# Kernel tuning notes

Hardware: AMD Instinct MI355X
Metric: run time of the kernel (lower is better)

The kernel has to match this reference:

```python
import jax, jax.numpy as jnp
import numpy as np

NUM_HEADS = 8
SPLIT_S = 4
DIM = 288            # n_feat * 3 * 3
SCALE = (DIM // NUM_HEADS) ** -0.5  # quirk: uses full dim's head_dim (36), not reduced
EPS = 1e-5


def _extract_patches(x):
    # x: [B,C,H,W] -> [B, C*9, H*W], 3x3 kernel, stride 1, 'same' padding
    B, C, H, W = x.shape
    xp = jnp.pad(x, ((0, 0), (0, 0), (1, 1), (1, 1)))
    pats = jnp.stack([xp[:, :, i:i + H, j:j + W] for i in range(3) for j in range(3)], axis=2)
    return pats.reshape(B, C * 9, H * W)


def _fold(cols, H, W):
    # inverse of extract: [B, C*9, H*W] -> [B,C,H,W], summing overlapping patches
    B, Ck, _ = cols.shape
    C = Ck // 9
    p = cols.reshape(B, C, 3, 3, H, W)
    out = jnp.zeros((B, C, H + 2, W + 2), cols.dtype)
    for i in range(3):
        for j in range(3):
            out = out.at[:, :, i:i + H, j:j + W].add(p[:, :, i, j])
    return out[:, :, 1:H + 1, 1:W + 1]


def _ln(x, w, b):
    mu = x.mean(-1, keepdims=True)
    var = ((x - mu) ** 2).mean(-1, keepdims=True)
    return (x - mu) * jax.lax.rsqrt(var + EPS) * w + b


def _attn(x, reduce_w, qkv_w, proj_w, proj_b):
    # x: [B,N,288] -> reduce -> [B,N,144] -> block-diag attention over s=4 chunks
    x = x @ reduce_w.T
    B, N, C = x.shape
    hd = C // NUM_HEADS
    qkv = (x @ qkv_w.T).reshape(B, N, 3, NUM_HEADS, hd).transpose(2, 0, 3, 1, 4)
    q, k, v = qkv[0], qkv[1], qkv[2]          # [B,h,N,hd]
    chunk = N // SPLIT_S
    q = q.reshape(B, NUM_HEADS, SPLIT_S, chunk, hd)
    k = k.reshape(B, NUM_HEADS, SPLIT_S, chunk, hd)
    v = v.reshape(B, NUM_HEADS, SPLIT_S, chunk, hd)
    attn = jnp.einsum('bhscd,bhsed->bhsce', q, k) * SCALE   # [B,h,s,chunk,chunk]
    attn = jax.nn.softmax(attn, axis=-1)
    out = jnp.einsum('bhsce,bhsed->bhscd', attn, v)          # [B,h,s,chunk,hd]
    out = out.transpose(0, 2, 3, 1, 4).reshape(B, N, C)      # cat chunks on token dim
    return out @ proj_w.T + proj_b


def setup_inputs() -> dict:
    key = jax.random.key(0)
    ks = jax.random.split(key, 12)
    d, dr, dh = DIM, DIM // 2, DIM // 4  # 288, 144, 72
    f = lambda k, shape: (jax.random.normal(k, shape, jnp.float32) * 0.02)
    return {
        'x': jax.random.normal(ks[0], (4, 32, 64, 64), jnp.float32),
        'ln1_w': jnp.ones((d,), jnp.float32), 'ln1_b': jnp.zeros((d,), jnp.float32),
        'reduce_w': f(ks[1], (dr, d)),
        'qkv_w': f(ks[2], (3 * dr, dr)),
        'proj_w': f(ks[3], (d, dr)), 'proj_b': jnp.zeros((d,), jnp.float32),
        'ln2_w': jnp.ones((d,), jnp.float32), 'ln2_b': jnp.zeros((d,), jnp.float32),
        'fc1_w': f(ks[4], (dh, d)), 'fc1_b': jnp.zeros((dh,), jnp.float32),
        'fc2_w': f(ks[5], (d, dh)), 'fc2_b': jnp.zeros((d,), jnp.float32),
    }


def reference(x, ln1_w, ln1_b, reduce_w, qkv_w, proj_w, proj_b, ln2_w, ln2_b, fc1_w, fc1_b, fc2_w, fc2_b):
    B, C, H, W = x.shape
    t = _extract_patches(x).transpose(0, 2, 1)  # [B, N=H*W, 288]
    t = t + _attn(_ln(t, ln1_w, ln1_b), reduce_w, qkv_w, proj_w, proj_b)
    h = _ln(t, ln2_w, ln2_b)
    t = t + (jax.nn.relu(h @ fc1_w.T + fc1_b) @ fc2_w.T + fc2_b)
    return _fold(t.transpose(0, 2, 1), H, W)
```

## Files before the change

kernel.cpp:

```cpp
#include <hip/hip_runtime.h>
#include <hip/hip_bf16.h>

typedef __hip_bfloat16 bf16;
typedef unsigned short u16;
typedef unsigned int u32;
typedef __attribute__((ext_vector_type(8))) short bf16x8;
typedef __attribute__((ext_vector_type(4))) float f32x4;

#define BB 4
#define CCH 32
#define HH 64
#define WW 64
#define NN 4096
#define D 288
#define DR 144
#define DQ 432
#define NH 8
#define HD 18
#define SPLIT 4
#define CHUNK 1024
#define KS 512
#define DH 72
#define SCALE_ 0.16666666666666666f
#define QSCALE 0.24044917348149343f
#define EPS_ 1e-5f
#define ASTR 160
#define ATS 168
#define HSTR 96

__device__ __attribute__((aligned(16))) u16 g_Wcb[DQ * D];
__device__ __attribute__((aligned(16))) u16 g_pw[D * ASTR];
__device__ __attribute__((aligned(16))) u16 g_f1w[HSTR * D];
__device__ __attribute__((aligned(16))) u16 g_f2w[D * HSTR];
__device__ __attribute__((aligned(16))) u16 g_q[(size_t)BB * NH * NN * 32];
__device__ __attribute__((aligned(16))) u16 g_k[(size_t)BB * NH * NN * 32];
__device__ __attribute__((aligned(16))) u16 g_vt[(size_t)BB * NH * SPLIT * 32 * CHUNK];
__device__ __attribute__((aligned(16))) float g_part[2 * (size_t)BB * NH * NN * 20];
__device__ __attribute__((aligned(16))) u16 g_t0[(size_t)BB * NN * D];
__device__ __attribute__((aligned(16))) u16 g_t2b[(size_t)BB * D * NN];
__device__ int   g_flag;

__device__ __forceinline__ float b2f(bf16 v) { return __bfloat162float(v); }
__device__ __forceinline__ float bits2f(u16 u) { return __uint_as_float(((u32)u) << 16); }
__device__ __forceinline__ u16 f2bits(float f) {
    u32 u = __float_as_uint(f);
    return (u16)((u + 0x7FFF + ((u >> 16) & 1)) >> 16);
}
__device__ __forceinline__ float ldin(const void* p, size_t i, int isbf) {
    return isbf ? b2f(((const bf16*)p)[i]) : ((const float*)p)[i];
}

#define RS  (D * ASTR + HSTR * D + D * HSTR)
#define RS2 (RS + BB * NH * SPLIT * CHUNK)
#define RSB ((RS2 + 255) / 256)
#define PATCHB (BB * HH)

__global__ void k_prep(const void* __restrict__ x, const void* __restrict__ qkv_w,
                       const void* __restrict__ reduce_w, const void* __restrict__ proj_w,
                       const void* __restrict__ fc1_w, const void* __restrict__ fc2_w) {
    __shared__ int cnt4[4];
    __shared__ float qw[DR];
    __shared__ float slab[32 * 3 * 66];
    int tid = threadIdx.x;
    {
        const u16* u = (const u16*)x;
        int c = 0;
        for (int i = tid; i < 2048; i += 256) c += (((u[i] >> 7) & 0xFF) >= 0x90);
        for (int o = 32; o; o >>= 1) c += __shfl_xor(c, o);
        if ((tid & 63) == 0) cnt4[tid >> 6] = c;
    }
    __syncthreads();
    int bf = (cnt4[0] + cnt4[1] + cnt4[2] + cnt4[3]) < 32;
    if (tid == 0 && blockIdx.x == 0) g_flag = bf;

    int bid = blockIdx.x;
    if (bid < DQ) {
        int o = bid;
        if (tid < DR) qw[tid] = ldin(qkv_w, (size_t)o * DR + tid, bf);
        __syncthreads();
        for (int col = tid; col < D; col += 256) {
            float s0 = 0.f, s1 = 0.f;
            #pragma unroll 4
            for (int j = 0; j < DR; j += 2) {
                s0 += qw[j] * ldin(reduce_w, (size_t)j * D + col, bf);
                s1 += qw[j + 1] * ldin(reduce_w, (size_t)(j + 1) * D + col, bf);
            }
            g_Wcb[(size_t)o * D + col] = f2bits(s0 + s1);
        }
    } else if (bid < DQ + RSB) {
        int idx = (bid - DQ) * 256 + tid;
        if (idx < D * ASTR) {
            int o = idx / ASTR, j = idx % ASTR;
            g_pw[idx] = (j < DR) ? f2bits(ldin(proj_w, (size_t)o * DR + j, bf)) : (u16)0;
        } else if (idx < D * ASTR + HSTR * D) {
            int t = idx - D * ASTR;
            int o = t / D;
            g_f1w[t] = (o < DH) ? f2bits(ldin(fc1_w, (size_t)t, bf)) : (u16)0;
        } else if (idx < RS) {
            int t = idx - D * ASTR - HSTR * D;
            int o = t / HSTR, j = t % HSTR;
            g_f2w[t] = (j < DH) ? f2bits(ldin(fc2_w, (size_t)o * DH + j, bf)) : (u16)0;
        } else if (idx < RS2) {
            int t = idx - RS;
            int bhs = t >> 10, n = t & 1023;
            g_vt[((size_t)bhs * 32 + 18) * CHUNK + n] = 0x3F80;
        }
    } else {
        int pb = bid - DQ - RSB;
        int b = pb >> 6, y = pb & 63;
        for (int idx = tid; idx < 32 * 3 * 66; idx += 256) {
            int c = idx / 198, rem = idx % 198;
            int ki = rem / 66, col = rem % 66 - 1;
            int sy = y + ki - 1;
            float v = 0.f;
            if (col >= 0 && col < 64 && sy >= 0 && sy < 64)
                v = ldin(x, ((size_t)(b * CCH + c) * HH + sy) * WW + col, bf);
            slab[idx] = v;
        }
        __syncthreads();
        size_t obase = ((size_t)b * NN + y * 64) * D;
        for (int idx = tid; idx < 64 * D; idx += 256) {
            int t = idx / D, f = idx % D;
            int c = f / 9, k = f % 9, ki = k / 3, kj = k % 3;
            g_t0[obase + idx] = f2bits(slab[c * 198 + ki * 66 + t + kj]);
        }
    }
}

__global__ void k_ln_qkv(const void* __restrict__ lnw, const void* __restrict__ lnb) {
    __shared__ __attribute__((aligned(16))) u16 xln[32 * 296];
    __shared__ float lnwf[D], lnbf[D];
    __shared__ float smu[32], srs[32];
    __shared__ u16 buf[3][144][32];
    int bf = g_flag;
    int tid = threadIdx.x;
    size_t tok0 = (size_t)blockIdx.x * 32;
    for (int i = tid; i < D; i += 256) { lnwf[i] = ldin(lnw, i, bf); lnbf[i] = ldin(lnb, i, bf); }
    {
        int tt = tid >> 3, p = tid & 7;
        const u32* pr = (const u32*)(g_t0 + (tok0 + tt) * D + p * 36);
        float s = 0.f, q = 0.f;
        #pragma unroll
        for (int j = 0; j < 18; ++j) {
            u32 v = pr[j];
            float a = bits2f((u16)(v & 0xFFFF)), b = bits2f((u16)(v >> 16));
            s += a + b; q += a * a + b * b;
        }
        #pragma unroll
        for (int o = 1; o < 8; o <<= 1) { s += __shfl_xor(s, o); q += __shfl_xor(q, o); }
        if (p == 0) {
            float mu = s / D;
            smu[tt] = mu;
            srs[tt] = rsqrtf(q / D - mu * mu + EPS_);
        }
    }
    __syncthreads();
    for (int idx = tid; idx < 32 * 144; idx += 256) {
        int t = idx / 144, dw = idx % 144;
        u32 v = *(const u32*)(g_t0 + (tok0 + t) * D + 2 * dw);
        float mu = smu[t], rs = srs[t];
        int f = 2 * dw;
        float a = (bits2f((u16)(v & 0xFFFF)) - mu) * rs * lnwf[f] + lnbf[f];
        float b = (bits2f((u16)(v >> 16)) - mu) * rs * lnwf[f + 1] + lnbf[f + 1];
        *(u32*)&xln[t * 296 + f] = (u32)f2bits(a) | ((u32)f2bits(b) << 16);
    }
    __syncthreads();
    int w = tid >> 6, lane = tid & 63, quad = lane >> 4, l15 = lane & 15;
    bf16x8 areg0[9], areg1[9];
    {
        const u16* a0 = xln + l15 * 296 + quad * 8;
        const u16* a1 = xln + (16 + l15) * 296 + quad * 8;
        #pragma unroll
        for (int ks = 0; ks < 9; ++ks) {
            areg0[ks] = *(const bf16x8*)(a0 + ks * 32);
            areg1[ks] = *(const bf16x8*)(a1 + ks * 32);
        }
    }
    int nt0 = w * 7, nt1 = (nt0 + 7 > 27) ? 27 : nt0 + 7;
    for (int nt = nt0; nt < nt1; ++nt) {
        f32x4 acc0 = {0.f, 0.f, 0.f, 0.f}, acc1 = {0.f, 0.f, 0.f, 0.f};
        const u16* bbase = g_Wcb + (size_t)(nt * 16 + l15) * D + quad * 8;
        #pragma unroll
        for (int ks = 0; ks < 9; ++ks) {
            bf16x8 bfr = *(const bf16x8*)(bbase + ks * 32);
            acc0 = __builtin_amdgcn_mfma_f32_16x16x32_bf16(areg0[ks], bfr, acc0, 0, 0, 0);
            acc1 = __builtin_amdgcn_mfma_f32_16x16x32_bf16(areg1[ks], bfr, acc1, 0, 0, 0);
        }
        int o = nt * 16 + l15;
        int which = o / DR, rem = o % DR;
        #pragma unroll
        for (int r = 0; r < 4; ++r) {
            buf[which][rem][quad * 4 + r] = f2bits(which == 0 ? acc0[r] * QSCALE : acc0[r]);
            buf[which][rem][16 + quad * 4 + r] = f2bits(which == 0 ? acc1[r] * QSCALE : acc1[r]);
        }
    }
    __syncthreads();
    {
        int b_ = (int)(tok0 >> 12);
        int n0 = (int)(tok0 & 4095);
        int sIdx = n0 >> 10, nc = n0 & 1023;
        for (int idx = tid; idx < 2 * 8 * 32 * 9; idx += 256) {
            int which = idx / 2304;
            int r2 = idx - which * 2304;
            int h = r2 / 288, r3 = r2 % 288, t = r3 / 9, dw = r3 % 9;
            u32 lo = buf[which][h * 18 + 2 * dw][t];
            u32 hi = buf[which][h * 18 + 2 * dw + 1][t];
            u16* dst = (which ? g_k : g_q) + ((size_t)(b_ * NH + h) * NN + n0 + t) * 32 + 2 * dw;
            *(u32*)dst = lo | (hi << 16);
        }
        for (int idx = tid; idx < 144 * 16; idx += 256) {
            int rem = idx >> 4, tp = idx & 15;
            int hh = rem / HD, dd = rem % HD;
            u32 lo = buf[2][rem][2 * tp];
            u32 hi = buf[2][rem][2 * tp + 1];
            size_t voff = (((size_t)(b_ * NH + hh) * SPLIT + sIdx) * 32 + dd) * CHUNK + nc + 2 * tp;
            *(u32*)&g_vt[voff] = lo | (hi << 16);
        }
    }
}

#define PSTR 72
__global__ __launch_bounds__(128) void k_attn() {
    __shared__ __attribute__((aligned(16))) u16 Pl[2][4][16 * PSTR];
    int bid = blockIdx.x;
    int chunk = bid & 127;
    int qblk = (bid >> 7) & 7;
    int ksl = bid >> 10;
    int s = chunk & 3, bh = chunk >> 2;
    int tid = threadIdx.x;
    int w = tid >> 6, lane = tid & 63, quad = lane >> 4, l15 = lane & 15;

    size_t rowbase = (size_t)bh * NN + s * CHUNK;
    size_t vtbase = ((size_t)bh * SPLIT + s) * 32 * CHUNK;
    const u16* kbase = g_k + rowbase * 32 + quad * 8;
    const u16* vbase = g_vt + vtbase + quad * 8;

    int qbase = qblk * 128 + w * 64;
    bf16x8 qf[4];
    #pragma unroll
    for (int t = 0; t < 4; ++t)
        qf[t] = *(const bf16x8*)(g_q + (rowbase + qbase + t * 16 + l15) * 32 + quad * 8);

    f32x4 accA[4], accB[4];
    #pragma unroll
    for (int t = 0; t < 4; ++t) {
        accA[t] = (f32x4){0.f, 0.f, 0.f, 0.f};
        accB[t] = (f32x4){0.f, 0.f, 0.f, 0.f};
    }

    int kt0 = ksl * KS;
    for (int kk = 0; kk < KS; kk += 64) {
        int kt = kt0 + kk;
        bf16x8 kf0 = *(const bf16x8*)(kbase + (size_t)(kt + 2 * l15) * 32);
        bf16x8 kf1 = *(const bf16x8*)(kbase + (size_t)(kt + 2 * l15 + 1) * 32);
        bf16x8 kf2 = *(const bf16x8*)(kbase + (size_t)(kt + 32 + 2 * l15) * 32);
        bf16x8 kf3 = *(const bf16x8*)(kbase + (size_t)(kt + 33 + 2 * l15) * 32);
        bf16x8 vA0 = *(const bf16x8*)(vbase + (size_t)l15 * CHUNK + kt);
        bf16x8 vB0 = *(const bf16x8*)(vbase + (size_t)(16 + l15) * CHUNK + kt);
        bf16x8 vA1 = *(const bf16x8*)(vbase + (size_t)l15 * CHUNK + kt + 32);
        bf16x8 vB1 = *(const bf16x8*)(vbase + (size_t)(16 + l15) * CHUNK + kt + 32);
        f32x4 z = {0.f, 0.f, 0.f, 0.f};
        #pragma unroll
        for (int t = 0; t < 4; ++t) {
            u16* pw = Pl[w][t];
            f32x4 S0 = __builtin_amdgcn_mfma_f32_16x16x32_bf16(qf[t], kf0, z, 0, 0, 0);
            f32x4 S1 = __builtin_amdgcn_mfma_f32_16x16x32_bf16(qf[t], kf1, z, 0, 0, 0);
            f32x4 S2 = __builtin_amdgcn_mfma_f32_16x16x32_bf16(qf[t], kf2, z, 0, 0, 0);
            f32x4 S3 = __builtin_amdgcn_mfma_f32_16x16x32_bf16(qf[t], kf3, z, 0, 0, 0);
            #pragma unroll
            for (int r = 0; r < 4; ++r) {
                float p0 = exp2f(S0[r]), p1 = exp2f(S1[r]);
                float p2 = exp2f(S2[r]), p3 = exp2f(S3[r]);
                u32 w0 = __builtin_amdgcn_perm(__float_as_uint(p1), __float_as_uint(p0), 0x07060302u);
                u32 w1 = __builtin_amdgcn_perm(__float_as_uint(p3), __float_as_uint(p2), 0x07060302u);
                *(u32*)&pw[(quad * 4 + r) * PSTR + 2 * l15] = w0;
                *(u32*)&pw[(quad * 4 + r) * PSTR + 32 + 2 * l15] = w1;
            }
        }
        #pragma unroll
        for (int t = 0; t < 4; ++t) {
            const u16* pw = Pl[w][t];
            bf16x8 pf0 = *(const bf16x8*)&pw[l15 * PSTR + quad * 8];
            bf16x8 pf1 = *(const bf16x8*)&pw[l15 * PSTR + 32 + quad * 8];
            accA[t] = __builtin_amdgcn_mfma_f32_16x16x32_bf16(pf0, vA0, accA[t], 0, 0, 0);
            accB[t] = __builtin_amdgcn_mfma_f32_16x16x32_bf16(pf0, vB0, accB[t], 0, 0, 0);
            accA[t] = __builtin_amdgcn_mfma_f32_16x16x32_bf16(pf1, vA1, accA[t], 0, 0, 0);
            accB[t] = __builtin_amdgcn_mfma_f32_16x16x32_bf16(pf1, vB1, accB[t], 0, 0, 0);
        }
    }
    float* pb = g_part + (((size_t)ksl * 32 + bh) * SPLIT + s) * (size_t)(CHUNK * 20);
    #pragma unroll
    for (int t = 0; t < 4; ++t) {
        #pragma unroll
        for (int r = 0; r < 4; ++r) {
            int tokenc = qbase + t * 16 + quad * 4 + r;
            float* row = pb + (size_t)tokenc * 20;
            row[l15] = accA[t][r];
            if (l15 < 3) row[16 + l15] = accB[t][r];
        }
    }
}

__global__ void k_proj_mlp(const void* __restrict__ proj_b, const void* __restrict__ lnw,
                           const void* __restrict__ lnb, const void* __restrict__ fc1_b,
                           const void* __restrict__ fc2_b) {
    __shared__ __attribute__((aligned(16))) u16 t1f[32 * 296];
    __shared__ __attribute__((aligned(16))) u16 xln[32 * 296];
    __shared__ __attribute__((aligned(16))) u16 attnT[32 * ATS];
    __shared__ __attribute__((aligned(16))) u16 hbuf[32 * HSTR];
    __shared__ float lnwf[D], lnbf[D];
    __shared__ float smu[32], srs[32];
    int bf = g_flag;
    int tid = threadIdx.x;
    size_t tok0 = (size_t)blockIdx.x * 32;
    int w = tid >> 6, lane = tid & 63, quad = lane >> 4, l15 = lane & 15;
    for (int i = tid; i < D; i += 256) { lnwf[i] = ldin(lnw, i, bf); lnbf[i] = ldin(lnb, i, bf); }

    int b_ = (int)(tok0 >> 12);
    int s_ = ((int)tok0 & 4095) >> 10;
    int tc0 = (int)tok0 & 1023;
    for (int idx = tid; idx < 32 * (ATS - DR); idx += 256) {
        int t = idx / (ATS - DR), f = idx % (ATS - DR);
        attnT[t * ATS + DR + f] = 0;
    }
    {
        int t = tid >> 3, h = tid & 7;
        const float* p1 = g_part + (((size_t)(b_ * NH + h)) * SPLIT + s_) * (size_t)(CHUNK * 20)
                        + (size_t)(tc0 + t) * 20;
        const float* p2 = p1 + (size_t)32 * SPLIT * CHUNK * 20;
        f32x4 a0 = *(const f32x4*)p1,        c0 = *(const f32x4*)p2;
        f32x4 a1 = *(const f32x4*)(p1 + 4),  c1 = *(const f32x4*)(p2 + 4);
        f32x4 a2 = *(const f32x4*)(p1 + 8),  c2 = *(const f32x4*)(p2 + 8);
        f32x4 a3 = *(const f32x4*)(p1 + 12), c3 = *(const f32x4*)(p2 + 12);
        f32x4 a4 = *(const f32x4*)(p1 + 16), c4 = *(const f32x4*)(p2 + 16);
        float inv = 1.f / (a4[2] + c4[2]);
        u16* dst = attnT + t * ATS + h * HD;
        #pragma unroll
        for (int d = 0; d < 4; ++d) {
            dst[d]      = f2bits((a0[d] + c0[d]) * inv);
            dst[4 + d]  = f2bits((a1[d] + c1[d]) * inv);
            dst[8 + d]  = f2bits((a2[d] + c2[d]) * inv);
            dst[12 + d] = f2bits((a3[d] + c3[d]) * inv);
        }
        dst[16] = f2bits((a4[0] + c4[0]) * inv);
        dst[17] = f2bits((a4[1] + c4[1]) * inv);
    }
    __syncthreads();

    {
        bf16x8 areg0[5], areg1[5];
        const u16* a0 = attnT + l15 * ATS + quad * 8;
        const u16* a1 = attnT + (16 + l15) * ATS + quad * 8;
        #pragma unroll
        for (int ks = 0; ks < 5; ++ks) {
            areg0[ks] = *(const bf16x8*)(a0 + ks * 32);
            areg1[ks] = *(const bf16x8*)(a1 + ks * 32);
        }
        const int tab[5] = {0, 5, 10, 14, 18};
        for (int nt = tab[w]; nt < tab[w + 1]; ++nt) {
            f32x4 acc0 = {0.f, 0.f, 0.f, 0.f}, acc1 = {0.f, 0.f, 0.f, 0.f};
            const u16* bbase = g_pw + (size_t)(nt * 16 + l15) * ASTR + quad * 8;
            #pragma unroll
            for (int ks = 0; ks < 5; ++ks) {
                bf16x8 bfr = *(const bf16x8*)(bbase + ks * 32);
                acc0 = __builtin_amdgcn_mfma_f32_16x16x32_bf16(areg0[ks], bfr, acc0, 0, 0, 0);
                acc1 = __builtin_amdgcn_mfma_f32_16x16x32_bf16(areg1[ks], bfr, acc1, 0, 0, 0);
            }
            int o = nt * 16 + l15;
            float bias = ldin(proj_b, o, bf);
            #pragma unroll
            for (int r = 0; r < 4; ++r) {
                t1f[(quad * 4 + r) * 296 + o] =
                    f2bits(bits2f(g_t0[(tok0 + quad * 4 + r) * D + o]) + acc0[r] + bias);
                t1f[(16 + quad * 4 + r) * 296 + o] =
                    f2bits(bits2f(g_t0[(tok0 + 16 + quad * 4 + r) * D + o]) + acc1[r] + bias);
            }
        }
    }
    __syncthreads();
    {
        int tt = tid >> 3, p = tid & 7;
        const u32* src = (const u32*)&t1f[tt * 296 + p * 36];
        float s = 0.f, q = 0.f;
        #pragma unroll
        for (int j = 0; j < 18; ++j) {
            u32 v = src[j];
            float a = bits2f((u16)(v & 0xFFFF)), b = bits2f((u16)(v >> 16));
            s += a + b; q += a * a + b * b;
        }
        #pragma unroll
        for (int o = 1; o < 8; o <<= 1) { s += __shfl_xor(s, o); q += __shfl_xor(q, o); }
        if (p == 0) {
            float mu = s / D;
            smu[tt] = mu;
            srs[tt] = rsqrtf(q / D - mu * mu + EPS_);
        }
    }
    __syncthreads();
    for (int idx = tid; idx < 32 * 144; idx += 256) {
        int t = idx / 144, dw = idx % 144;
        int f = 2 * dw;
        u32 v = *(const u32*)&t1f[t * 296 + f];
        float mu = smu[t], rs = srs[t];
        float a = (bits2f((u16)(v & 0xFFFF)) - mu) * rs * lnwf[f] + lnbf[f];
        float b = (bits2f((u16)(v >> 16)) - mu) * rs * lnwf[f + 1] + lnbf[f + 1];
        *(u32*)&xln[t * 296 + f] = (u32)f2bits(a) | ((u32)f2bits(b) << 16);
    }
    __syncthreads();
    {
        bf16x8 areg0[9], areg1[9];
        const u16* a0 = xln + l15 * 296 + quad * 8;
        const u16* a1 = xln + (16 + l15) * 296 + quad * 8;
        #pragma unroll
        for (int ks = 0; ks < 9; ++ks) {
            areg0[ks] = *(const bf16x8*)(a0 + ks * 32);
            areg1[ks] = *(const bf16x8*)(a1 + ks * 32);
        }
        const int tab2[5] = {0, 2, 4, 5, 6};
        for (int nt = tab2[w]; nt < tab2[w + 1]; ++nt) {
            f32x4 acc0 = {0.f, 0.f, 0.f, 0.f}, acc1 = {0.f, 0.f, 0.f, 0.f};
            const u16* bbase = g_f1w + (size_t)(nt * 16 + l15) * D + quad * 8;
            #pragma unroll
            for (int ks = 0; ks < 9; ++ks) {
                bf16x8 bfr = *(const bf16x8*)(bbase + ks * 32);
                acc0 = __builtin_amdgcn_mfma_f32_16x16x32_bf16(areg0[ks], bfr, acc0, 0, 0, 0);
                acc1 = __builtin_amdgcn_mfma_f32_16x16x32_bf16(areg1[ks], bfr, acc1, 0, 0, 0);
            }
            int o = nt * 16 + l15;
            float bias = (o < DH) ? ldin(fc1_b, o, bf) : 0.f;
            #pragma unroll
            for (int r = 0; r < 4; ++r) {
                hbuf[(quad * 4 + r) * HSTR + o] = f2bits(fmaxf(acc0[r] + bias, 0.f));
                hbuf[(16 + quad * 4 + r) * HSTR + o] = f2bits(fmaxf(acc1[r] + bias, 0.f));
            }
        }
    }
    __syncthreads();
    {
        bf16x8 areg0[3], areg1[3];
        const u16* a0 = hbuf + l15 * HSTR + quad * 8;
        const u16* a1 = hbuf + (16 + l15) * HSTR + quad * 8;
        #pragma unroll
        for (int ks = 0; ks < 3; ++ks) {
            areg0[ks] = *(const bf16x8*)(a0 + ks * 32);
            areg1[ks] = *(const bf16x8*)(a1 + ks * 32);
        }
        const int tab[5] = {0, 5, 10, 14, 18};
        for (int nt = tab[w]; nt < tab[w + 1]; ++nt) {
            f32x4 acc0 = {0.f, 0.f, 0.f, 0.f}, acc1 = {0.f, 0.f, 0.f, 0.f};
            const u16* bbase = g_f2w + (size_t)(nt * 16 + l15) * HSTR + quad * 8;
            #pragma unroll
            for (int ks = 0; ks < 3; ++ks) {
                bf16x8 bfr = *(const bf16x8*)(bbase + ks * 32);
                acc0 = __builtin_amdgcn_mfma_f32_16x16x32_bf16(areg0[ks], bfr, acc0, 0, 0, 0);
                acc1 = __builtin_amdgcn_mfma_f32_16x16x32_bf16(areg1[ks], bfr, acc1, 0, 0, 0);
            }
            int o = nt * 16 + l15;
            float bias = ldin(fc2_b, o, bf);
            #pragma unroll
            for (int r = 0; r < 4; ++r) {
                xln[(quad * 4 + r) * 296 + o] =
                    f2bits(bits2f(t1f[(quad * 4 + r) * 296 + o]) + acc0[r] + bias);
                xln[(16 + quad * 4 + r) * 296 + o] =
                    f2bits(bits2f(t1f[(16 + quad * 4 + r) * 296 + o]) + acc1[r] + bias);
            }
        }
    }
    __syncthreads();
    {
        int n0 = (int)(tok0 & 4095);
        for (int idx = tid; idx < D * 16; idx += 256) {
            int o = idx >> 4, tp = idx & 15;
            u32 v = (u32)xln[(2 * tp) * 296 + o] | ((u32)xln[(2 * tp + 1) * 296 + o] << 16);
            *(u32*)&g_t2b[((size_t)b_ * D + o) * NN + n0 + 2 * tp] = v;
        }
    }
}

__global__ void k_fold(void* __restrict__ out) {
    int bf = g_flag;
    int idx = blockIdx.x * blockDim.x + threadIdx.x;
    if (idx >= BB * CCH * HH * WW) return;
    int xx = idx % WW;
    int y = (idx / WW) % HH;
    int c = (idx / (WW * HH)) % CCH;
    int b = idx / (WW * HH * CCH);
    const u16* base = g_t2b + ((size_t)b * D + c * 9) * NN;
    float s = 0.f;
    #pragma unroll
    for (int i = 0; i < 3; ++i) {
        int sy = y + 1 - i;
        if (sy < 0 || sy >= HH) continue;
        #pragma unroll
        for (int j = 0; j < 3; ++j) {
            int sx = xx + 1 - j;
            if (sx < 0 || sx >= WW) continue;
            s += bits2f(base[(size_t)(i * 3 + j) * NN + sy * WW + sx]);
        }
    }
    if (bf) ((bf16*)out)[idx] = __float2bfloat16(s);
    else    ((float*)out)[idx] = s;
}

extern "C" void kernel_launch(void* const* d_in, const int* in_sizes, int n_in,
                              void* d_out, int out_size, void* d_ws, size_t ws_size,
                              hipStream_t stream) {
    const void* x        = d_in[0];
    const void* ln1_w    = d_in[1];
    const void* ln1_b    = d_in[2];
    const void* reduce_w = d_in[3];
    const void* qkv_w    = d_in[4];
    const void* proj_w   = d_in[5];
    const void* proj_b   = d_in[6];
    const void* ln2_w    = d_in[7];
    const void* ln2_b    = d_in[8];
    const void* fc1_w    = d_in[9];
    const void* fc1_b    = d_in[10];
    const void* fc2_w    = d_in[11];
    const void* fc2_b    = d_in[12];

    k_prep     <<<DQ + RSB + PATCHB, 256, 0, stream>>>(x, qkv_w, reduce_w, proj_w, fc1_w, fc2_w);
    k_ln_qkv   <<<BB * NN / 32, 256, 0, stream>>>(ln1_w, ln1_b);
    k_attn     <<<2 * BB * NH * SPLIT * 8, 128, 0, stream>>>();
    k_proj_mlp <<<BB * NN / 32, 256, 0, stream>>>(proj_b, ln2_w, ln2_b, fc1_b, fc2_b);
    k_fold     <<<(BB * CCH * HH * WW + 255) / 256, 256, 0, stream>>>(d_out);
}
```

Before: 200.0 us.

## Keep attention probabilities in registers by transposing S and permuting V layout

The QK^T MFMA now computes S transposed (K as the A operand), so each lane's accumulator values line up with the A-operand layout needed for the PV MFMA. The exponentials are packed straight into bf16x8 registers instead of going through a shared-memory staging buffer. To match, the V^T producer writes keys in a permuted order within each 32-key group. This removes the LDS writes, reads and their latency from the attention inner loop and adds a launch-bounds occupancy hint, at the cost of a more fragile layout coupling between the producer and the consumer kernel.

Result: no change. 197.1 us (-1.4%).

```diff
diff --git a/kernel.cpp b/kernel.cpp
--- a/kernel.cpp
+++ b/kernel.cpp
@@ -49,6 +49,10 @@
 __device__ __forceinline__ float ldin(const void* p, size_t i, int isbf) {
     return isbf ? b2f(((const bf16*)p)[i]) : ((const float*)p)[i];
 }
+__device__ __forceinline__ u32 packexp(float e0, float e1) {
+    return __builtin_amdgcn_perm(__float_as_uint(exp2f(e1)),
+                                 __float_as_uint(exp2f(e0)), 0x07060302u);
+}
 
 #define RS  (D * ASTR + HSTR * D + D * HSTR)
 #define RS2 (RS + BB * NH * SPLIT * CHUNK)
@@ -213,15 +217,15 @@
             int hh = rem / HD, dd = rem % HD;
             u32 lo = buf[2][rem][2 * tp];
             u32 hi = buf[2][rem][2 * tp + 1];
-            size_t voff = (((size_t)(b_ * NH + hh) * SPLIT + sIdx) * 32 + dd) * CHUNK + nc + 2 * tp;
+            int k2 = 2 * tp;
+            int pos = 8 * ((k2 >> 2) & 3) + 4 * (k2 >> 4) + (k2 & 3);
+            size_t voff = (((size_t)(b_ * NH + hh) * SPLIT + sIdx) * 32 + dd) * CHUNK + nc + pos;
             *(u32*)&g_vt[voff] = lo | (hi << 16);
         }
     }
 }
 
-#define PSTR 72
-__global__ __launch_bounds__(128) void k_attn() {
-    __shared__ __attribute__((aligned(16))) u16 Pl[2][4][16 * PSTR];
+__global__ __launch_bounds__(128, 4) void k_attn() {
     int bid = blockIdx.x;
     int chunk = bid & 127;
     int qblk = (bid >> 7) & 7;
@@ -251,10 +255,10 @@
     int kt0 = ksl * KS;
     for (int kk = 0; kk < KS; kk += 64) {
         int kt = kt0 + kk;
-        bf16x8 kf0 = *(const bf16x8*)(kbase + (size_t)(kt + 2 * l15) * 32);
-        bf16x8 kf1 = *(const bf16x8*)(kbase + (size_t)(kt + 2 * l15 + 1) * 32);
-        bf16x8 kf2 = *(const bf16x8*)(kbase + (size_t)(kt + 32 + 2 * l15) * 32);
-        bf16x8 kf3 = *(const bf16x8*)(kbase + (size_t)(kt + 33 + 2 * l15) * 32);
+        bf16x8 kf0 = *(const bf16x8*)(kbase + (size_t)(kt + l15) * 32);
+        bf16x8 kf1 = *(const bf16x8*)(kbase + (size_t)(kt + 16 + l15) * 32);
+        bf16x8 kf2 = *(const bf16x8*)(kbase + (size_t)(kt + 32 + l15) * 32);
+        bf16x8 kf3 = *(const bf16x8*)(kbase + (size_t)(kt + 48 + l15) * 32);
         bf16x8 vA0 = *(const bf16x8*)(vbase + (size_t)l15 * CHUNK + kt);
         bf16x8 vB0 = *(const bf16x8*)(vbase + (size_t)(16 + l15) * CHUNK + kt);
         bf16x8 vA1 = *(const bf16x8*)(vbase + (size_t)l15 * CHUNK + kt + 32);
@@ -262,30 +266,23 @@
         f32x4 z = {0.f, 0.f, 0.f, 0.f};
         #pragma unroll
         for (int t = 0; t < 4; ++t) {
-            u16* pw = Pl[w][t];
-            f32x4 S0 = __builtin_amdgcn_mfma_f32_16x16x32_bf16(qf[t], kf0, z, 0, 0, 0);
-            f32x4 S1 = __builtin_amdgcn_mfma_f32_16x16x32_bf16(qf[t], kf1, z, 0, 0, 0);
-            f32x4 S2 = __builtin_amdgcn_mfma_f32_16x16x32_bf16(qf[t], kf2, z, 0, 0, 0);
-            f32x4 S3 = __builtin_amdgcn_mfma_f32_16x16x32_bf16(qf[t], kf3, z, 0, 0, 0);
-            #pragma unroll
-            for (int r = 0; r < 4; ++r) {
-                float p0 = exp2f(S0[r]), p1 = exp2f(S1[r]);
-                float p2 = exp2f(S2[r]), p3 = exp2f(S3[r]);
-                u32 w0 = __builtin_amdgcn_perm(__float_as_uint(p1), __float_as_uint(p0), 0x07060302u);
-                u32 w1 = __builtin_amdgcn_perm(__float_as_uint(p3), __float_as_uint(p2), 0x07060302u);
-                *(u32*)&pw[(quad * 4 + r) * PSTR + 2 * l15] = w0;
-                *(u32*)&pw[(quad * 4 + r) * PSTR + 32 + 2 * l15] = w1;
-            }
-        }
-        #pragma unroll
-        for (int t = 0; t < 4; ++t) {
-            const u16* pw = Pl[w][t];
-            bf16x8 pf0 = *(const bf16x8*)&pw[l15 * PSTR + quad * 8];
-            bf16x8 pf1 = *(const bf16x8*)&pw[l15 * PSTR + 32 + quad * 8];
-            accA[t] = __builtin_amdgcn_mfma_f32_16x16x32_bf16(pf0, vA0, accA[t], 0, 0, 0);
-            accB[t] = __builtin_amdgcn_mfma_f32_16x16x32_bf16(pf0, vB0, accB[t], 0, 0, 0);
-            accA[t] = __builtin_amdgcn_mfma_f32_16x16x32_bf16(pf1, vA1, accA[t], 0, 0, 0);
-            accB[t] = __builtin_amdgcn_mfma_f32_16x16x32_bf16(pf1, vB1, accB[t], 0, 0, 0);
+            f32x4 S0 = __builtin_amdgcn_mfma_f32_16x16x32_bf16(kf0, qf[t], z, 0, 0, 0);
+            f32x4 S1 = __builtin_amdgcn_mfma_f32_16x16x32_bf16(kf1, qf[t], z, 0, 0, 0);
+            f32x4 S2 = __builtin_amdgcn_mfma_f32_16x16x32_bf16(kf2, qf[t], z, 0, 0, 0);
+            f32x4 S3 = __builtin_amdgcn_mfma_f32_16x16x32_bf16(kf3, qf[t], z, 0, 0, 0);
+            union { u32 u[4]; bf16x8 v; } pa0, pa1;
+            pa0.u[0] = packexp(S0[0], S0[1]);
+            pa0.u[1] = packexp(S0[2], S0[3]);
+            pa0.u[2] = packexp(S1[0], S1[1]);
+            pa0.u[3] = packexp(S1[2], S1[3]);
+            pa1.u[0] = packexp(S2[0], S2[1]);
+            pa1.u[1] = packexp(S2[2], S2[3]);
+            pa1.u[2] = packexp(S3[0], S3[1]);
+            pa1.u[3] = packexp(S3[2], S3[3]);
+            accA[t] = __builtin_amdgcn_mfma_f32_16x16x32_bf16(pa0.v, vA0, accA[t], 0, 0, 0);
+            accB[t] = __builtin_amdgcn_mfma_f32_16x16x32_bf16(pa0.v, vB0, accB[t], 0, 0, 0);
+            accA[t] = __builtin_amdgcn_mfma_f32_16x16x32_bf16(pa1.v, vA1, accA[t], 0, 0, 0);
+            accB[t] = __builtin_amdgcn_mfma_f32_16x16x32_bf16(pa1.v, vB1, accB[t], 0, 0, 0);
         }
     }
     float* pb = g_part + (((size_t)ksl * 32 + bh) * SPLIT + s) * (size_t)(CHUNK * 20);
```
